# Kernel optimization log

Measured on AMD Instinct MI355X. Metric: run time of the kernel, lower is better.

## Reference

```python
import jax, jax.numpy as jnp
import numpy as np

L1 = 0.05
L2 = 0.05
L3 = 0.05
L4 = 0.05
D_MIN = 1.0
EPS = 1e-12


def _pairwise_dist(x, y):
    sq = (jnp.sum(x * x, axis=-1)[:, None]
          + jnp.sum(y * y, axis=-1)[None, :]
          - 2.0 * (x @ y.T))
    return jnp.sqrt(jnp.clip(sq, EPS))


def setup_inputs() -> dict:
    key = jax.random.key(0)
    k1, k2, k3, k4, k5, k6 = jax.random.split(key, 6)
    B, C, D, d, P = 32768, 100, 1024, 512, 128
    return {
        "predictions": jax.random.normal(k1, (B, C), dtype=jnp.float32),
        "reconstructions": jax.random.normal(k2, (B, D), dtype=jnp.float32),
        "data": jax.random.normal(k3, (B, D), dtype=jnp.float32),
        "embeddings": jax.random.normal(k4, (B, d), dtype=jnp.float32),
        "prototypes": jax.random.normal(k5, (P, d), dtype=jnp.float32),
        "labels": jax.random.randint(k6, (B,), 0, C, dtype=jnp.int64),
    }


def reference(predictions, reconstructions, data, embeddings, prototypes, labels):
    B = predictions.shape[0]
    P = prototypes.shape[0]

    # Cross-entropy (mean reduction, class-index targets)
    logp = jax.nn.log_softmax(predictions, axis=-1)
    classification_loss = -jnp.mean(logp[jnp.arange(B), labels])

    # MSE reconstruction loss (mean reduction)
    reconstruction_loss = jnp.mean((reconstructions - data) ** 2)

    # Prototype diversity penalty: sum_{j<k} max(0, d_min - ||p_j - p_k||)^2
    proto_dist = _pairwise_dist(prototypes, prototypes)  # [P, P]
    hinge = jnp.maximum(0.0, D_MIN - proto_dist) ** 2
    upper = jnp.triu(jnp.ones((P, P), dtype=bool), k=1)
    diversity_penalty = jnp.sum(jnp.where(upper, hinge, 0.0))

    # Embedding-to-prototype distances [B, P], shared by similarity/coverage penalties
    dist = _pairwise_dist(embeddings, prototypes)
    similarity_penalty = jnp.sum(jnp.min(dist, axis=0)) / P
    coverage_penalty = jnp.sum(jnp.min(dist, axis=1)) / B

    total_loss = (classification_loss
                  + L1 * reconstruction_loss
                  + L2 * diversity_penalty
                  + L3 * similarity_penalty
                  + L4 * coverage_penalty)
    return total_loss
```

## Files before the change

### kernel.cpp

```cpp
#include <hip/hip_runtime.h>
#include <hip/hip_bf16.h>


constexpr float FEPS = 1e-12f;
constexpr float DMIN = 1.0f;

#define NB_DIST 512
#define NB_MSE  1024
#define NB_CE   256
#define NB_DIV  128

typedef unsigned short ushort_t;
typedef __attribute__((ext_vector_type(8))) short bf16x8;
typedef __attribute__((ext_vector_type(8))) unsigned short u16x8;
typedef __attribute__((ext_vector_type(4))) unsigned short u16x4;
typedef __attribute__((ext_vector_type(16))) float f32x16;
typedef __attribute__((ext_vector_type(4))) float f32x4;

typedef __attribute__((address_space(1))) const void gvoid_t;
typedef __attribute__((address_space(3))) void lvoid_t;

__device__ __forceinline__ unsigned short f2b(float f) {
    unsigned u = __float_as_uint(f);
    u += 0x7FFFu + ((u >> 16) & 1u);
    return (unsigned short)(u >> 16);
}

union SmemU {
    struct {
        char     As[8192];
        char     Bs[16384];
        float    rown[64];
        float    pn[128];
        unsigned rowmin[64];
        unsigned colmin[128];
    } dist;
    struct { float pp[512]; float spp; float sred[4]; } div;
    struct { float sred[4]; } red;
};

__global__ __launch_bounds__(128) void conv_kernel(const float* __restrict__ proto,
                                                   ushort_t* __restrict__ pB,
                                                   float* __restrict__ pnorm,
                                                   float* __restrict__ ws,
                                                   unsigned* __restrict__ proto_min) {
    int p = blockIdx.x, q = threadIdx.x;
    if (q == 0) proto_min[p] = 0x7F7F7F7Fu;
    if (p == 0 && q < 4) ws[q] = 0.f;
    float4 v = ((const float4*)(proto + (size_t)p * 512))[q];
    u16x4 o = { f2b(v.x), f2b(v.y), f2b(v.z), f2b(v.w) };
    *(u16x4*)(pB + (size_t)p * 512 + q * 4) = o;
    float s = v.x * v.x + v.y * v.y + v.z * v.z + v.w * v.w;
    #pragma unroll
    for (int off = 32; off; off >>= 1) s += __shfl_xor(s, off);
    __shared__ float sr[2];
    if ((q & 63) == 0) sr[q >> 6] = s;
    __syncthreads();
    if (q == 0) pnorm[p] = sr[0] + sr[1];
}

__device__ __forceinline__ void dist_body_fast(SmemU& sm, int bid,
                                               const float* __restrict__ emb,
                                               const ushort_t* __restrict__ pB,
                                               const float* __restrict__ pnormG,
                                               unsigned* __restrict__ proto_min,
                                               float* __restrict__ cov_out) {
    char*     AsB     = sm.dist.As;
    char*     BsB     = sm.dist.Bs;
    float*    rownL   = sm.dist.rown;
    float*    pnL     = sm.dist.pn;
    unsigned* rowminL = sm.dist.rowmin;
    unsigned* colminL = sm.dist.colmin;

    const int t  = threadIdx.x;
    const int m0 = bid * 64;

    if (t < 64)  { rownL[t] = 0.f; rowminL[t] = 0x7F7F7F7Fu; }
    if (t < 128) { colminL[t] = 0x7F7F7F7Fu; pnL[t] = pnormG[t]; }

    int aidx[4], rowi[4], swzi[4];
    const float4* embF4 = (const float4*)emb;
    #pragma unroll
    for (int i = 0; i < 4; ++i) {
        int flat = i * 256 + t;
        int row = flat >> 4, colq = flat & 15;
        rowi[i] = row;
        aidx[i] = (m0 + row) * 128 + colq;
        swzi[i] = row * 128 + ((((colq >> 1) ^ (row & 7)) << 4) | ((colq & 1) << 3));
    }

    const ushort_t* bsrcp[4];
    char* bdstW[4];
    #pragma unroll
    for (int i = 0; i < 4; ++i) {
        int f = i * 256 + t;
        int pr = f >> 3, gb = f & 7;
        bsrcp[i] = pB + pr * 512 + ((gb ^ (pr & 7)) << 3);
        bdstW[i] = BsB + (size_t)(i * 256 + (t & ~63)) * 16;
    }

    const int lane = t & 63, wv = t >> 6;
    const int wr = wv >> 1, wc = wv & 1;
    const int lo = lane & 31, hi = lane >> 5;
    const int arow = wr * 32 + lo;
    const int arz  = arow & 7;
    const int p0 = wc * 64 + lo, p1 = p0 + 32;
    const int pz = p0 & 7;
    const char* Ar  = AsB + arow * 128;
    const char* Br0 = BsB + p0 * 128;
    const char* Br1 = BsB + p1 * 128;

    float4 aE0 = embF4[aidx[0]], aE1 = embF4[aidx[1]],
           aE2 = embF4[aidx[2]], aE3 = embF4[aidx[3]];
    float4 aO0, aO1, aO2, aO3;
    float rn0 = 0.f, rn1 = 0.f, rn2 = 0.f, rn3 = 0.f;
    f32x16 acc0 = {}, acc1 = {};
    __syncthreads();

#define DIST_CHUNK(c, W0, W1, W2, W3, L0, L1, L2, L3)                          \
    {                                                                          \
        const int kc = (c) * 64;                                               \
        __builtin_amdgcn_global_load_lds((gvoid_t*)(bsrcp[0] + kc),            \
                                         (lvoid_t*)bdstW[0], 16, 0, 0);        \
        __builtin_amdgcn_global_load_lds((gvoid_t*)(bsrcp[1] + kc),            \
                                         (lvoid_t*)bdstW[1], 16, 0, 0);        \
        __builtin_amdgcn_global_load_lds((gvoid_t*)(bsrcp[2] + kc),            \
                                         (lvoid_t*)bdstW[2], 16, 0, 0);        \
        __builtin_amdgcn_global_load_lds((gvoid_t*)(bsrcp[3] + kc),            \
                                         (lvoid_t*)bdstW[3], 16, 0, 0);        \
        __builtin_amdgcn_sched_barrier(0);                                     \
        {                                                                      \
            const int kn = ((c) < 7 ? (c) + 1 : 7) * 16;                       \
            L0 = embF4[aidx[0] + kn]; L1 = embF4[aidx[1] + kn];                \
            L2 = embF4[aidx[2] + kn]; L3 = embF4[aidx[3] + kn];                \
        }                                                                      \
        __builtin_amdgcn_sched_barrier(0);                                     \
        rn0 = fmaf(W0.x, W0.x, rn0); rn0 = fmaf(W0.y, W0.y, rn0);              \
        rn0 = fmaf(W0.z, W0.z, rn0); rn0 = fmaf(W0.w, W0.w, rn0);              \
        rn1 = fmaf(W1.x, W1.x, rn1); rn1 = fmaf(W1.y, W1.y, rn1);              \
        rn1 = fmaf(W1.z, W1.z, rn1); rn1 = fmaf(W1.w, W1.w, rn1);              \
        rn2 = fmaf(W2.x, W2.x, rn2); rn2 = fmaf(W2.y, W2.y, rn2);              \
        rn2 = fmaf(W2.z, W2.z, rn2); rn2 = fmaf(W2.w, W2.w, rn2);              \
        rn3 = fmaf(W3.x, W3.x, rn3); rn3 = fmaf(W3.y, W3.y, rn3);              \
        rn3 = fmaf(W3.z, W3.z, rn3); rn3 = fmaf(W3.w, W3.w, rn3);              \
        { u16x4 u = { f2b(W0.x), f2b(W0.y), f2b(W0.z), f2b(W0.w) };            \
          *(u16x4*)(AsB + swzi[0]) = u; }                                      \
        { u16x4 u = { f2b(W1.x), f2b(W1.y), f2b(W1.z), f2b(W1.w) };            \
          *(u16x4*)(AsB + swzi[1]) = u; }                                      \
        { u16x4 u = { f2b(W2.x), f2b(W2.y), f2b(W2.z), f2b(W2.w) };            \
          *(u16x4*)(AsB + swzi[2]) = u; }                                      \
        { u16x4 u = { f2b(W3.x), f2b(W3.y), f2b(W3.z), f2b(W3.w) };            \
          *(u16x4*)(AsB + swzi[3]) = u; }                                      \
        asm volatile("s_waitcnt vmcnt(4)" ::: "memory");                       \
        asm volatile("s_waitcnt lgkmcnt(0)" ::: "memory");                     \
        __builtin_amdgcn_s_barrier();                                          \
        __builtin_amdgcn_sched_barrier(0);                                     \
        _Pragma("unroll")                                                      \
        for (int s = 0; s < 4; ++s) {                                          \
            const int g = (s * 2 + hi);                                        \
            bf16x8 af = *(const bf16x8*)(Ar  + ((g ^ arz) << 4));              \
            bf16x8 b0 = *(const bf16x8*)(Br0 + ((g ^ pz)  << 4));              \
            bf16x8 b1 = *(const bf16x8*)(Br1 + ((g ^ pz)  << 4));              \
            acc0 = __builtin_amdgcn_mfma_f32_32x32x16_bf16(af, b0, acc0, 0,0,0); \
            acc1 = __builtin_amdgcn_mfma_f32_32x32x16_bf16(af, b1, acc1, 0,0,0); \
        }                                                                      \
        asm volatile("s_waitcnt lgkmcnt(0)" ::: "memory");                     \
        __builtin_amdgcn_s_barrier();                                          \
        __builtin_amdgcn_sched_barrier(0);                                     \
    }

    #pragma unroll
    for (int c = 0; c < 8; c += 2) {
        DIST_CHUNK(c,     aE0, aE1, aE2, aE3, aO0, aO1, aO2, aO3)
        DIST_CHUNK(c + 1, aO0, aO1, aO2, aO3, aE0, aE1, aE2, aE3)
    }
#undef DIST_CHUNK

    atomicAdd(&rownL[rowi[0]], rn0);
    atomicAdd(&rownL[rowi[1]], rn1);
    atomicAdd(&rownL[rowi[2]], rn2);
    atomicAdd(&rownL[rowi[3]], rn3);
    __syncthreads();

    const float pn0 = pnL[p0], pn1 = pnL[p1];
    float cmin0 = 3.0e38f, cmin1 = 3.0e38f;
    #pragma unroll
    for (int r = 0; r < 16; ++r) {
        const int row = wr * 32 + (r & 3) + 8 * (r >> 2) + 4 * hi;
        const float nx = rownL[row];
        float d0 = sqrtf(fmaxf(nx + pn0 - 2.f * acc0[r], FEPS));
        float d1 = sqrtf(fmaxf(nx + pn1 - 2.f * acc1[r], FEPS));
        cmin0 = fminf(cmin0, d0);
        cmin1 = fminf(cmin1, d1);
        atomicMin(&rowminL[row], __float_as_uint(fminf(d0, d1)));
    }
    atomicMin(&colminL[p0], __float_as_uint(cmin0));
    atomicMin(&colminL[p1], __float_as_uint(cmin1));
    __syncthreads();

    if (t < 64) {
        float cv = __uint_as_float(rowminL[t]);
        #pragma unroll
        for (int o = 32; o; o >>= 1) cv += __shfl_xor(cv, o);
        if (t == 0) atomicAdd(cov_out, cv);
    }
    if (t < 128) atomicMin(&proto_min[t], colminL[t]);
}

__device__ __forceinline__ void dist_body_slow(SmemU& sm, int bid,
                                               const float* __restrict__ emb,
                                               const float* __restrict__ proto,
                                               unsigned* __restrict__ proto_min,
                                               float* __restrict__ cov_out) {
    char*     AsB     = sm.dist.As;
    char*     BsB     = sm.dist.Bs;
    float*    rownL   = sm.dist.rown;
    float*    pnL     = sm.dist.pn;
    unsigned* rowminL = sm.dist.rowmin;
    unsigned* colminL = sm.dist.colmin;

    const int t  = threadIdx.x;
    const int m0 = bid * 64;

    if (t < 64)  { rownL[t] = 0.f; rowminL[t] = 0x7F7F7F7Fu; }
    if (t < 128) { colminL[t] = 0x7F7F7F7Fu; pnL[t] = 0.f; }
    __syncthreads();

    const int ra = t >> 2, qa = t & 3;
    const int pb = t >> 1, hb = t & 1;
    const int raz = ra & 7, pbz = pb & 7;

    const float4* aG  = (const float4*)(emb + (size_t)(m0 + ra) * 512 + qa * 16);
    const float4* bGf = (const float4*)(proto + (size_t)pb * 512 + hb * 32);

    const int lane = t & 63, wv = t >> 6;
    const int wr = wv >> 1, wc = wv & 1;
    const int lo = lane & 31, hi = lane >> 5;
    const int arow = wr * 32 + lo;
    const int arz  = arow & 7;
    const int p0 = wc * 64 + lo, p1 = p0 + 32;
    const int pz = p0 & 7;

    float4 av0 = aG[0], av1 = aG[1], av2 = aG[2], av3 = aG[3];
    float4 bf0 = bGf[0], bf1 = bGf[1], bf2 = bGf[2], bf3 = bGf[3],
           bf4 = bGf[4], bf5 = bGf[5], bf6 = bGf[6], bf7 = bGf[7];

    f32x16 acc0 = {}, acc1 = {};
    char* Aw = AsB + ra * 128;
    char* Bw = BsB + pb * 128;
    const char* Ar  = AsB + arow * 128;
    const char* Br0 = BsB + p0 * 128;
    const char* Br1 = BsB + p1 * 128;

    for (int c = 0; c < 8; ++c) {
        {
            float nx = 0.f;
            nx = fmaf(av0.x, av0.x, nx); nx = fmaf(av0.y, av0.y, nx);
            nx = fmaf(av0.z, av0.z, nx); nx = fmaf(av0.w, av0.w, nx);
            nx = fmaf(av1.x, av1.x, nx); nx = fmaf(av1.y, av1.y, nx);
            nx = fmaf(av1.z, av1.z, nx); nx = fmaf(av1.w, av1.w, nx);
            nx = fmaf(av2.x, av2.x, nx); nx = fmaf(av2.y, av2.y, nx);
            nx = fmaf(av2.z, av2.z, nx); nx = fmaf(av2.w, av2.w, nx);
            nx = fmaf(av3.x, av3.x, nx); nx = fmaf(av3.y, av3.y, nx);
            nx = fmaf(av3.z, av3.z, nx); nx = fmaf(av3.w, av3.w, nx);
            atomicAdd(&rownL[ra], nx);
            u16x8 w0 = { f2b(av0.x), f2b(av0.y), f2b(av0.z), f2b(av0.w),
                         f2b(av1.x), f2b(av1.y), f2b(av1.z), f2b(av1.w) };
            u16x8 w1 = { f2b(av2.x), f2b(av2.y), f2b(av2.z), f2b(av2.w),
                         f2b(av3.x), f2b(av3.y), f2b(av3.z), f2b(av3.w) };
            *(u16x8*)(Aw + (((qa * 2 + 0) ^ raz) << 4)) = w0;
            *(u16x8*)(Aw + (((qa * 2 + 1) ^ raz) << 4)) = w1;

            float pns = 0.f;
            pns = fmaf(bf0.x, bf0.x, pns); pns = fmaf(bf0.y, bf0.y, pns);
            pns = fmaf(bf0.z, bf0.z, pns); pns = fmaf(bf0.w, bf0.w, pns);
            pns = fmaf(bf1.x, bf1.x, pns); pns = fmaf(bf1.y, bf1.y, pns);
            pns = fmaf(bf1.z, bf1.z, pns); pns = fmaf(bf1.w, bf1.w, pns);
            pns = fmaf(bf2.x, bf2.x, pns); pns = fmaf(bf2.y, bf2.y, pns);
            pns = fmaf(bf2.z, bf2.z, pns); pns = fmaf(bf2.w, bf2.w, pns);
            pns = fmaf(bf3.x, bf3.x, pns); pns = fmaf(bf3.y, bf3.y, pns);
            pns = fmaf(bf3.z, bf3.z, pns); pns = fmaf(bf3.w, bf3.w, pns);
            pns = fmaf(bf4.x, bf4.x, pns); pns = fmaf(bf4.y, bf4.y, pns);
            pns = fmaf(bf4.z, bf4.z, pns); pns = fmaf(bf4.w, bf4.w, pns);
            pns = fmaf(bf5.x, bf5.x, pns); pns = fmaf(bf5.y, bf5.y, pns);
            pns = fmaf(bf5.z, bf5.z, pns); pns = fmaf(bf5.w, bf5.w, pns);
            pns = fmaf(bf6.x, bf6.x, pns); pns = fmaf(bf6.y, bf6.y, pns);
            pns = fmaf(bf6.z, bf6.z, pns); pns = fmaf(bf6.w, bf6.w, pns);
            pns = fmaf(bf7.x, bf7.x, pns); pns = fmaf(bf7.y, bf7.y, pns);
            pns = fmaf(bf7.z, bf7.z, pns); pns = fmaf(bf7.w, bf7.w, pns);
            atomicAdd(&pnL[pb], pns);
            u16x8 x0 = { f2b(bf0.x), f2b(bf0.y), f2b(bf0.z), f2b(bf0.w),
                         f2b(bf1.x), f2b(bf1.y), f2b(bf1.z), f2b(bf1.w) };
            u16x8 x1 = { f2b(bf2.x), f2b(bf2.y), f2b(bf2.z), f2b(bf2.w),
                         f2b(bf3.x), f2b(bf3.y), f2b(bf3.z), f2b(bf3.w) };
            u16x8 x2 = { f2b(bf4.x), f2b(bf4.y), f2b(bf4.z), f2b(bf4.w),
                         f2b(bf5.x), f2b(bf5.y), f2b(bf5.z), f2b(bf5.w) };
            u16x8 x3 = { f2b(bf6.x), f2b(bf6.y), f2b(bf6.z), f2b(bf6.w),
                         f2b(bf7.x), f2b(bf7.y), f2b(bf7.z), f2b(bf7.w) };
            *(u16x8*)(Bw + (((hb * 4 + 0) ^ pbz) << 4)) = x0;
            *(u16x8*)(Bw + (((hb * 4 + 1) ^ pbz) << 4)) = x1;
            *(u16x8*)(Bw + (((hb * 4 + 2) ^ pbz) << 4)) = x2;
            *(u16x8*)(Bw + (((hb * 4 + 3) ^ pbz) << 4)) = x3;
        }
        __syncthreads();
        if (c < 7) {
            av0 = aG[(c + 1) * 16 + 0]; av1 = aG[(c + 1) * 16 + 1];
            av2 = aG[(c + 1) * 16 + 2]; av3 = aG[(c + 1) * 16 + 3];
            bf0 = bGf[(c + 1) * 16 + 0]; bf1 = bGf[(c + 1) * 16 + 1];
            bf2 = bGf[(c + 1) * 16 + 2]; bf3 = bGf[(c + 1) * 16 + 3];
            bf4 = bGf[(c + 1) * 16 + 4]; bf5 = bGf[(c + 1) * 16 + 5];
            bf6 = bGf[(c + 1) * 16 + 6]; bf7 = bGf[(c + 1) * 16 + 7];
        }
        #pragma unroll
        for (int s = 0; s < 4; ++s) {
            const int g = (s * 2 + hi);
            bf16x8 af = *(const bf16x8*)(Ar  + ((g ^ arz) << 4));
            bf16x8 b0 = *(const bf16x8*)(Br0 + ((g ^ pz)  << 4));
            bf16x8 b1 = *(const bf16x8*)(Br1 + ((g ^ pz)  << 4));
            acc0 = __builtin_amdgcn_mfma_f32_32x32x16_bf16(af, b0, acc0, 0, 0, 0);
            acc1 = __builtin_amdgcn_mfma_f32_32x32x16_bf16(af, b1, acc1, 0, 0, 0);
        }
        __syncthreads();
    }

    const float pn0 = pnL[p0], pn1 = pnL[p1];
    float cmin0 = 3.0e38f, cmin1 = 3.0e38f;
    #pragma unroll
    for (int r = 0; r < 16; ++r) {
        const int row = wr * 32 + (r & 3) + 8 * (r >> 2) + 4 * hi;
        const float nx = rownL[row];
        float d0 = sqrtf(fmaxf(nx + pn0 - 2.f * acc0[r], FEPS));
        float d1 = sqrtf(fmaxf(nx + pn1 - 2.f * acc1[r], FEPS));
        cmin0 = fminf(cmin0, d0);
        cmin1 = fminf(cmin1, d1);
        atomicMin(&rowminL[row], __float_as_uint(fminf(d0, d1)));
    }
    atomicMin(&colminL[p0], __float_as_uint(cmin0));
    atomicMin(&colminL[p1], __float_as_uint(cmin1));
    __syncthreads();

    if (t < 64) {
        float cv = __uint_as_float(rowminL[t]);
        #pragma unroll
        for (int o = 32; o; o >>= 1) cv += __shfl_xor(cv, o);
        if (t == 0) atomicAdd(cov_out, cv);
    }
    if (t < 128) atomicMin(&proto_min[t], colminL[t]);
}

__device__ __forceinline__ void mse_body(SmemU& sm, int mb,
                                         const float4* __restrict__ r,
                                         const float4* __restrict__ d,
                                         float* __restrict__ out, int n4) {
    const int t  = threadIdx.x;
    const int CH = (n4 + NB_MSE - 1) / NB_MSE;
    const int base = mb * CH;
    const int L = (base + CH <= n4) ? CH : (n4 - base);
    const f32x4* rb = (const f32x4*)(r + base);
    const f32x4* db = (const f32x4*)(d + base);
    float acc0 = 0.f, acc1 = 0.f, acc2 = 0.f, acc3 = 0.f;
    int k = t;
    for (; k + 7 * 256 < L; k += 8 * 256) {
        f32x4 a0 = __builtin_nontemporal_load(&rb[k + 0 * 256]);
        f32x4 a1 = __builtin_nontemporal_load(&rb[k + 1 * 256]);
        f32x4 a2 = __builtin_nontemporal_load(&rb[k + 2 * 256]);
        f32x4 a3 = __builtin_nontemporal_load(&rb[k + 3 * 256]);
        f32x4 a4 = __builtin_nontemporal_load(&rb[k + 4 * 256]);
        f32x4 a5 = __builtin_nontemporal_load(&rb[k + 5 * 256]);
        f32x4 a6 = __builtin_nontemporal_load(&rb[k + 6 * 256]);
        f32x4 a7 = __builtin_nontemporal_load(&rb[k + 7 * 256]);
        f32x4 b0 = __builtin_nontemporal_load(&db[k + 0 * 256]);
        f32x4 b1 = __builtin_nontemporal_load(&db[k + 1 * 256]);
        f32x4 b2 = __builtin_nontemporal_load(&db[k + 2 * 256]);
        f32x4 b3 = __builtin_nontemporal_load(&db[k + 3 * 256]);
        f32x4 b4 = __builtin_nontemporal_load(&db[k + 4 * 256]);
        f32x4 b5 = __builtin_nontemporal_load(&db[k + 5 * 256]);
        f32x4 b6 = __builtin_nontemporal_load(&db[k + 6 * 256]);
        f32x4 b7 = __builtin_nontemporal_load(&db[k + 7 * 256]);
        f32x4 e;
        e = a0 - b0; acc0 = fmaf(e.x, e.x, acc0); acc1 = fmaf(e.y, e.y, acc1);
                     acc2 = fmaf(e.z, e.z, acc2); acc3 = fmaf(e.w, e.w, acc3);
        e = a1 - b1; acc0 = fmaf(e.x, e.x, acc0); acc1 = fmaf(e.y, e.y, acc1);
                     acc2 = fmaf(e.z, e.z, acc2); acc3 = fmaf(e.w, e.w, acc3);
        e = a2 - b2; acc0 = fmaf(e.x, e.x, acc0); acc1 = fmaf(e.y, e.y, acc1);
                     acc2 = fmaf(e.z, e.z, acc2); acc3 = fmaf(e.w, e.w, acc3);
        e = a3 - b3; acc0 = fmaf(e.x, e.x, acc0); acc1 = fmaf(e.y, e.y, acc1);
                     acc2 = fmaf(e.z, e.z, acc2); acc3 = fmaf(e.w, e.w, acc3);
        e = a4 - b4; acc0 = fmaf(e.x, e.x, acc0); acc1 = fmaf(e.y, e.y, acc1);
                     acc2 = fmaf(e.z, e.z, acc2); acc3 = fmaf(e.w, e.w, acc3);
        e = a5 - b5; acc0 = fmaf(e.x, e.x, acc0); acc1 = fmaf(e.y, e.y, acc1);
                     acc2 = fmaf(e.z, e.z, acc2); acc3 = fmaf(e.w, e.w, acc3);
        e = a6 - b6; acc0 = fmaf(e.x, e.x, acc0); acc1 = fmaf(e.y, e.y, acc1);
                     acc2 = fmaf(e.z, e.z, acc2); acc3 = fmaf(e.w, e.w, acc3);
        e = a7 - b7; acc0 = fmaf(e.x, e.x, acc0); acc1 = fmaf(e.y, e.y, acc1);
                     acc2 = fmaf(e.z, e.z, acc2); acc3 = fmaf(e.w, e.w, acc3);
    }
    for (; k < L; k += 256) {
        f32x4 a = __builtin_nontemporal_load(&rb[k]);
        f32x4 b = __builtin_nontemporal_load(&db[k]);
        f32x4 e = a - b;
        acc0 = fmaf(e.x, e.x, acc0); acc1 = fmaf(e.y, e.y, acc1);
        acc2 = fmaf(e.z, e.z, acc2); acc3 = fmaf(e.w, e.w, acc3);
    }
    float acc = (acc0 + acc1) + (acc2 + acc3);
    #pragma unroll
    for (int o = 32; o; o >>= 1) acc += __shfl_xor(acc, o);
    int lane = t & 63, w = t >> 6;
    if (lane == 0) sm.red.sred[w] = acc;
    __syncthreads();
    if (t == 0) atomicAdd(out, sm.red.sred[0] + sm.red.sred[1]
                             + sm.red.sred[2] + sm.red.sred[3]);
}

__device__ __forceinline__ void ce_body(SmemU& sm, int cb,
                                        const float* __restrict__ pred,
                                        const int* __restrict__ lab,
                                        float* __restrict__ ce_out,
                                        int B, int C) {
    const int rows_per_wave = B / (NB_CE * 4);
    int lane = threadIdx.x & 63;
    int w    = threadIdx.x >> 6;
    int wid  = cb * 4 + w;
    float acc = 0.f;
    for (int i = 0; i < rows_per_wave; ++i) {
        int row = wid * rows_per_wave + i;
        const float* p = pred + (size_t)row * C;
        float v1 = (lane < C)      ? p[lane]      : -3.0e38f;
        float v2 = (lane + 64 < C) ? p[lane + 64] : -3.0e38f;
        float m = fmaxf(v1, v2);
        #pragma unroll
        for (int o = 32; o; o >>= 1) m = fmaxf(m, __shfl_xor(m, o));
        float s = ((lane < C) ? __expf(v1 - m) : 0.f)
                + ((lane + 64 < C) ? __expf(v2 - m) : 0.f);
        #pragma unroll
        for (int o = 32; o; o >>= 1) s += __shfl_xor(s, o);
        float lv = p[lab[row]];
        acc += m + __logf(s) - lv;
    }
    if (lane == 0) sm.red.sred[w] = acc;
    __syncthreads();
    if (threadIdx.x == 0) atomicAdd(ce_out, sm.red.sred[0] + sm.red.sred[1]
                                          + sm.red.sred[2] + sm.red.sred[3]);
}

__device__ __forceinline__ void div_body(SmemU& sm, int p,
                                         const float* __restrict__ proto,
                                         float* __restrict__ div_out, int dd) {
    int q = threadIdx.x;
    bool act = q < 128;
    if (act) for (int k = q; k < dd; k += 128) sm.div.pp[k] = proto[(size_t)p * dd + k];
    __syncthreads();
    float dot = 0.f, qq = 0.f;
    if (act) {
        const float4* pq4 = (const float4*)(proto + (size_t)q * dd);
        const float4* pp4 = (const float4*)sm.div.pp;
        for (int k4 = 0; k4 < dd / 4; ++k4) {
            float4 v = pq4[k4];
            float4 u = pp4[k4];
            dot = fmaf(u.x, v.x, dot); dot = fmaf(u.y, v.y, dot);
            dot = fmaf(u.z, v.z, dot); dot = fmaf(u.w, v.w, dot);
            qq  = fmaf(v.x, v.x, qq);  qq  = fmaf(v.y, v.y, qq);
            qq  = fmaf(v.z, v.z, qq);  qq  = fmaf(v.w, v.w, qq);
        }
        if (q == p) sm.div.spp = qq;
    }
    __syncthreads();
    float h2 = 0.f;
    if (act && q > p) {
        float sq = sm.div.spp + qq - 2.f * dot;
        float dist = sqrtf(fmaxf(sq, FEPS));
        float h = fmaxf(0.f, DMIN - dist);
        h2 = h * h;
    }
    #pragma unroll
    for (int o = 32; o; o >>= 1) h2 += __shfl_xor(h2, o);
    if ((q & 63) == 0) sm.div.sred[q >> 6] = h2;
    __syncthreads();
    if (q == 0) atomicAdd(div_out, sm.div.sred[0] + sm.div.sred[1]
                                 + sm.div.sred[2] + sm.div.sred[3]);
}

template<bool PRECONV>
__global__ __launch_bounds__(256, 4) void fused_kernel(
        const float* __restrict__ pred, const int* __restrict__ lab,
        const float4* __restrict__ recon4, const float4* __restrict__ data4,
        const float* __restrict__ emb, const float* __restrict__ proto,
        const ushort_t* __restrict__ pB, const float* __restrict__ pnormG,
        float* __restrict__ ws, unsigned* __restrict__ proto_min,
        int B, int C, int n4, int dd) {
    __shared__ __attribute__((aligned(16))) SmemU sm;
    int bid = blockIdx.x;
    if (bid < NB_DIST) {
        if constexpr (PRECONV)
            dist_body_fast(sm, bid, emb, pB, pnormG, proto_min, ws + 3);
        else
            dist_body_slow(sm, bid, emb, proto, proto_min, ws + 3);
    } else if (bid < NB_DIST + NB_MSE) {
        mse_body(sm, bid - NB_DIST, recon4, data4, ws + 1, n4);
    } else if (bid < NB_DIST + NB_MSE + NB_CE) {
        ce_body(sm, bid - NB_DIST - NB_MSE, pred, lab, ws + 0, B, C);
    } else {
        div_body(sm, bid - NB_DIST - NB_MSE - NB_CE, proto, ws + 2, dd);
    }
}

__global__ void final_kernel(const float* __restrict__ ws,
                             const unsigned* __restrict__ pmin,
                             float* __restrict__ out, int B, int D, int P) {
    float sim = 0.f;
    for (int i = 0; i < P; ++i) sim += __uint_as_float(pmin[i]);
    float ce  = ws[0] / (float)B;
    float mse = ws[1] / ((float)B * (float)D);
    out[0] = ce + 0.05f * mse + 0.05f * ws[2] + 0.05f * (sim / (float)P)
           + 0.05f * (ws[3] / (float)B);
}

extern "C" void kernel_launch(void* const* d_in, const int* in_sizes, int n_in,
                              void* d_out, int out_size, void* d_ws, size_t ws_size,
                              hipStream_t stream) {
    const float* pred  = (const float*)d_in[0];
    const float* recon = (const float*)d_in[1];
    const float* data  = (const float*)d_in[2];
    const float* emb   = (const float*)d_in[3];
    const float* proto = (const float*)d_in[4];
    const int*   lab   = (const int*)d_in[5];
    float* out = (float*)d_out;

    int B  = in_sizes[5];
    int C  = in_sizes[0] / B;
    int D  = in_sizes[1] / B;
    int dd = in_sizes[3] / B;
    int P  = in_sizes[4] / dd;

    float* ws = (float*)d_ws;
    unsigned* proto_min = (unsigned*)(ws + 4);
    float*    pnorm     = ws + 132;
    ushort_t* pB        = (ushort_t*)((char*)d_ws + 1280);
    bool preconv = ws_size >= (size_t)(1280 + 128 * 512 * 2);

    int n4 = (B * D) / 4;
    int grid = NB_DIST + NB_MSE + NB_CE + NB_DIV;
    if (preconv) {
        conv_kernel<<<128, 128, 0, stream>>>(proto, pB, pnorm, ws, proto_min);
        fused_kernel<true><<<grid, 256, 0, stream>>>(
            pred, lab, (const float4*)recon, (const float4*)data, emb, proto,
            pB, pnorm, ws, proto_min, B, C, n4, dd);
    } else {
        hipMemsetAsync(ws, 0, 4 * sizeof(float), stream);
        hipMemsetAsync(ws + 4, 0x7F, P * sizeof(unsigned), stream);
        fused_kernel<false><<<grid, 256, 0, stream>>>(
            pred, lab, (const float4*)recon, (const float4*)data, emb, proto,
            nullptr, nullptr, ws, proto_min, B, C, n4, dd);
    }
    final_kernel<<<1, 1, 0, stream>>>(ws, proto_min, out, B, D, P);
}
```

Baseline: 104.1 us.

## Halve distance blocks with two tiles each, drop nontemporal loads and occupancy hint

Distance work now runs on 256 blocks that each process two consecutive tiles, with a barrier between them. This cuts block count and moves the distance blocks' share of the fused grid toward the MSE streaming blocks. The MSE loads become ordinary cached loads instead of nontemporal ones, and the launch-bounds minimum-occupancy hint is removed, letting the compiler use more registers. The risks are lower occupancy and a longer serial critical path for the distance blocks.

```diff
diff --git a/kernel.cpp b/kernel.cpp
--- a/kernel.cpp
+++ b/kernel.cpp
@@ -5,7 +5,7 @@
 constexpr float FEPS = 1e-12f;
 constexpr float DMIN = 1.0f;
 
-#define NB_DIST 512
+#define NB_DIST 256
 #define NB_MSE  1024
 #define NB_CE   256
 #define NB_DIV  128
@@ -361,22 +361,22 @@
     float acc0 = 0.f, acc1 = 0.f, acc2 = 0.f, acc3 = 0.f;
     int k = t;
     for (; k + 7 * 256 < L; k += 8 * 256) {
-        f32x4 a0 = __builtin_nontemporal_load(&rb[k + 0 * 256]);
-        f32x4 a1 = __builtin_nontemporal_load(&rb[k + 1 * 256]);
-        f32x4 a2 = __builtin_nontemporal_load(&rb[k + 2 * 256]);
-        f32x4 a3 = __builtin_nontemporal_load(&rb[k + 3 * 256]);
-        f32x4 a4 = __builtin_nontemporal_load(&rb[k + 4 * 256]);
-        f32x4 a5 = __builtin_nontemporal_load(&rb[k + 5 * 256]);
-        f32x4 a6 = __builtin_nontemporal_load(&rb[k + 6 * 256]);
-        f32x4 a7 = __builtin_nontemporal_load(&rb[k + 7 * 256]);
-        f32x4 b0 = __builtin_nontemporal_load(&db[k + 0 * 256]);
-        f32x4 b1 = __builtin_nontemporal_load(&db[k + 1 * 256]);
-        f32x4 b2 = __builtin_nontemporal_load(&db[k + 2 * 256]);
-        f32x4 b3 = __builtin_nontemporal_load(&db[k + 3 * 256]);
-        f32x4 b4 = __builtin_nontemporal_load(&db[k + 4 * 256]);
-        f32x4 b5 = __builtin_nontemporal_load(&db[k + 5 * 256]);
-        f32x4 b6 = __builtin_nontemporal_load(&db[k + 6 * 256]);
-        f32x4 b7 = __builtin_nontemporal_load(&db[k + 7 * 256]);
+        f32x4 a0 = rb[k + 0 * 256];
+        f32x4 a1 = rb[k + 1 * 256];
+        f32x4 a2 = rb[k + 2 * 256];
+        f32x4 a3 = rb[k + 3 * 256];
+        f32x4 a4 = rb[k + 4 * 256];
+        f32x4 a5 = rb[k + 5 * 256];
+        f32x4 a6 = rb[k + 6 * 256];
+        f32x4 a7 = rb[k + 7 * 256];
+        f32x4 b0 = db[k + 0 * 256];
+        f32x4 b1 = db[k + 1 * 256];
+        f32x4 b2 = db[k + 2 * 256];
+        f32x4 b3 = db[k + 3 * 256];
+        f32x4 b4 = db[k + 4 * 256];
+        f32x4 b5 = db[k + 5 * 256];
+        f32x4 b6 = db[k + 6 * 256];
+        f32x4 b7 = db[k + 7 * 256];
         f32x4 e;
         e = a0 - b0; acc0 = fmaf(e.x, e.x, acc0); acc1 = fmaf(e.y, e.y, acc1);
                      acc2 = fmaf(e.z, e.z, acc2); acc3 = fmaf(e.w, e.w, acc3);
@@ -396,8 +396,8 @@
                      acc2 = fmaf(e.z, e.z, acc2); acc3 = fmaf(e.w, e.w, acc3);
     }
     for (; k < L; k += 256) {
-        f32x4 a = __builtin_nontemporal_load(&rb[k]);
-        f32x4 b = __builtin_nontemporal_load(&db[k]);
+        f32x4 a = rb[k];
+        f32x4 b = db[k];
         f32x4 e = a - b;
         acc0 = fmaf(e.x, e.x, acc0); acc1 = fmaf(e.y, e.y, acc1);
         acc2 = fmaf(e.z, e.z, acc2); acc3 = fmaf(e.w, e.w, acc3);
@@ -481,7 +481,7 @@
 }
 
 template<bool PRECONV>
-__global__ __launch_bounds__(256, 4) void fused_kernel(
+__global__ __launch_bounds__(256) void fused_kernel(
         const float* __restrict__ pred, const int* __restrict__ lab,
         const float4* __restrict__ recon4, const float4* __restrict__ data4,
         const float* __restrict__ emb, const float* __restrict__ proto,
@@ -491,10 +491,15 @@
     __shared__ __attribute__((aligned(16))) SmemU sm;
     int bid = blockIdx.x;
     if (bid < NB_DIST) {
-        if constexpr (PRECONV)
-            dist_body_fast(sm, bid, emb, pB, pnormG, proto_min, ws + 3);
-        else
-            dist_body_slow(sm, bid, emb, proto, proto_min, ws + 3);
+        if constexpr (PRECONV) {
+            dist_body_fast(sm, bid * 2, emb, pB, pnormG, proto_min, ws + 3);
+            __syncthreads();
+            dist_body_fast(sm, bid * 2 + 1, emb, pB, pnormG, proto_min, ws + 3);
+        } else {
+            dist_body_slow(sm, bid * 2, emb, proto, proto_min, ws + 3);
+            __syncthreads();
+            dist_body_slow(sm, bid * 2 + 1, emb, proto, proto_min, ws + 3);
+        }
     } else if (bid < NB_DIST + NB_MSE) {
         mse_body(sm, bid - NB_DIST, recon4, data4, ws + 1, n4);
     } else if (bid < NB_DIST + NB_MSE + NB_CE) {
```

New measurement: 120.4 us. 1.16x slower.

## Split MSE reduction into its own kernel with more blocks

Applied to the files above, without the earlier changes.

Moves the MSE reduction out of the heterogeneous fused kernel into a separate lightweight kernel launched after the distance/CE/diversity kernel. The MSE kernel uses only a tiny shared array, so it no longer inherits the large shared-memory union and register footprint, which should allow higher occupancy for the bandwidth-bound streaming. The block count for MSE also doubles. The cost is an extra launch and that MSE no longer overlaps with the dist work in the same grid.

```diff
diff --git a/kernel.cpp b/kernel.cpp
--- a/kernel.cpp
+++ b/kernel.cpp
@@ -6,7 +6,7 @@
 constexpr float DMIN = 1.0f;
 
 #define NB_DIST 512
-#define NB_MSE  1024
+#define NB_MSE  2048
 #define NB_CE   256
 #define NB_DIV  128
 
@@ -348,70 +348,6 @@
     if (t < 128) atomicMin(&proto_min[t], colminL[t]);
 }
 
-__device__ __forceinline__ void mse_body(SmemU& sm, int mb,
-                                         const float4* __restrict__ r,
-                                         const float4* __restrict__ d,
-                                         float* __restrict__ out, int n4) {
-    const int t  = threadIdx.x;
-    const int CH = (n4 + NB_MSE - 1) / NB_MSE;
-    const int base = mb * CH;
-    const int L = (base + CH <= n4) ? CH : (n4 - base);
-    const f32x4* rb = (const f32x4*)(r + base);
-    const f32x4* db = (const f32x4*)(d + base);
-    float acc0 = 0.f, acc1 = 0.f, acc2 = 0.f, acc3 = 0.f;
-    int k = t;
-    for (; k + 7 * 256 < L; k += 8 * 256) {
-        f32x4 a0 = __builtin_nontemporal_load(&rb[k + 0 * 256]);
-        f32x4 a1 = __builtin_nontemporal_load(&rb[k + 1 * 256]);
-        f32x4 a2 = __builtin_nontemporal_load(&rb[k + 2 * 256]);
-        f32x4 a3 = __builtin_nontemporal_load(&rb[k + 3 * 256]);
-        f32x4 a4 = __builtin_nontemporal_load(&rb[k + 4 * 256]);
-        f32x4 a5 = __builtin_nontemporal_load(&rb[k + 5 * 256]);
-        f32x4 a6 = __builtin_nontemporal_load(&rb[k + 6 * 256]);
-        f32x4 a7 = __builtin_nontemporal_load(&rb[k + 7 * 256]);
-        f32x4 b0 = __builtin_nontemporal_load(&db[k + 0 * 256]);
-        f32x4 b1 = __builtin_nontemporal_load(&db[k + 1 * 256]);
-        f32x4 b2 = __builtin_nontemporal_load(&db[k + 2 * 256]);
-        f32x4 b3 = __builtin_nontemporal_load(&db[k + 3 * 256]);
-        f32x4 b4 = __builtin_nontemporal_load(&db[k + 4 * 256]);
-        f32x4 b5 = __builtin_nontemporal_load(&db[k + 5 * 256]);
-        f32x4 b6 = __builtin_nontemporal_load(&db[k + 6 * 256]);
-        f32x4 b7 = __builtin_nontemporal_load(&db[k + 7 * 256]);
-        f32x4 e;
-        e = a0 - b0; acc0 = fmaf(e.x, e.x, acc0); acc1 = fmaf(e.y, e.y, acc1);
-                     acc2 = fmaf(e.z, e.z, acc2); acc3 = fmaf(e.w, e.w, acc3);
-        e = a1 - b1; acc0 = fmaf(e.x, e.x, acc0); acc1 = fmaf(e.y, e.y, acc1);
-                     acc2 = fmaf(e.z, e.z, acc2); acc3 = fmaf(e.w, e.w, acc3);
-        e = a2 - b2; acc0 = fmaf(e.x, e.x, acc0); acc1 = fmaf(e.y, e.y, acc1);
-                     acc2 = fmaf(e.z, e.z, acc2); acc3 = fmaf(e.w, e.w, acc3);
-        e = a3 - b3; acc0 = fmaf(e.x, e.x, acc0); acc1 = fmaf(e.y, e.y, acc1);
-                     acc2 = fmaf(e.z, e.z, acc2); acc3 = fmaf(e.w, e.w, acc3);
-        e = a4 - b4; acc0 = fmaf(e.x, e.x, acc0); acc1 = fmaf(e.y, e.y, acc1);
-                     acc2 = fmaf(e.z, e.z, acc2); acc3 = fmaf(e.w, e.w, acc3);
-        e = a5 - b5; acc0 = fmaf(e.x, e.x, acc0); acc1 = fmaf(e.y, e.y, acc1);
-                     acc2 = fmaf(e.z, e.z, acc2); acc3 = fmaf(e.w, e.w, acc3);
-        e = a6 - b6; acc0 = fmaf(e.x, e.x, acc0); acc1 = fmaf(e.y, e.y, acc1);
-                     acc2 = fmaf(e.z, e.z, acc2); acc3 = fmaf(e.w, e.w, acc3);
-        e = a7 - b7; acc0 = fmaf(e.x, e.x, acc0); acc1 = fmaf(e.y, e.y, acc1);
-                     acc2 = fmaf(e.z, e.z, acc2); acc3 = fmaf(e.w, e.w, acc3);
-    }
-    for (; k < L; k += 256) {
-        f32x4 a = __builtin_nontemporal_load(&rb[k]);
-        f32x4 b = __builtin_nontemporal_load(&db[k]);
-        f32x4 e = a - b;
-        acc0 = fmaf(e.x, e.x, acc0); acc1 = fmaf(e.y, e.y, acc1);
-        acc2 = fmaf(e.z, e.z, acc2); acc3 = fmaf(e.w, e.w, acc3);
-    }
-    float acc = (acc0 + acc1) + (acc2 + acc3);
-    #pragma unroll
-    for (int o = 32; o; o >>= 1) acc += __shfl_xor(acc, o);
-    int lane = t & 63, w = t >> 6;
-    if (lane == 0) sm.red.sred[w] = acc;
-    __syncthreads();
-    if (t == 0) atomicAdd(out, sm.red.sred[0] + sm.red.sred[1]
-                             + sm.red.sred[2] + sm.red.sred[3]);
-}
-
 __device__ __forceinline__ void ce_body(SmemU& sm, int cb,
                                         const float* __restrict__ pred,
                                         const int* __restrict__ lab,
@@ -481,13 +417,12 @@
 }
 
 template<bool PRECONV>
-__global__ __launch_bounds__(256, 4) void fused_kernel(
+__global__ __launch_bounds__(256) void dcd_kernel(
         const float* __restrict__ pred, const int* __restrict__ lab,
-        const float4* __restrict__ recon4, const float4* __restrict__ data4,
         const float* __restrict__ emb, const float* __restrict__ proto,
         const ushort_t* __restrict__ pB, const float* __restrict__ pnormG,
         float* __restrict__ ws, unsigned* __restrict__ proto_min,
-        int B, int C, int n4, int dd) {
+        int B, int C, int dd) {
     __shared__ __attribute__((aligned(16))) SmemU sm;
     int bid = blockIdx.x;
     if (bid < NB_DIST) {
@@ -495,13 +430,74 @@
             dist_body_fast(sm, bid, emb, pB, pnormG, proto_min, ws + 3);
         else
             dist_body_slow(sm, bid, emb, proto, proto_min, ws + 3);
-    } else if (bid < NB_DIST + NB_MSE) {
-        mse_body(sm, bid - NB_DIST, recon4, data4, ws + 1, n4);
-    } else if (bid < NB_DIST + NB_MSE + NB_CE) {
-        ce_body(sm, bid - NB_DIST - NB_MSE, pred, lab, ws + 0, B, C);
+    } else if (bid < NB_DIST + NB_CE) {
+        ce_body(sm, bid - NB_DIST, pred, lab, ws + 0, B, C);
     } else {
-        div_body(sm, bid - NB_DIST - NB_MSE - NB_CE, proto, ws + 2, dd);
-    }
+        div_body(sm, bid - NB_DIST - NB_CE, proto, ws + 2, dd);
+    }
+}
+
+__global__ __launch_bounds__(256) void mse_kernel(const f32x4* __restrict__ r,
+                                                  const f32x4* __restrict__ d,
+                                                  float* __restrict__ out, int n4) {
+    __shared__ float sred[4];
+    const int t  = threadIdx.x;
+    const int CH = (n4 + NB_MSE - 1) / NB_MSE;
+    const int base = blockIdx.x * CH;
+    const int L = (base + CH <= n4) ? CH : (n4 - base);
+    const f32x4* rb = r + base;
+    const f32x4* db = d + base;
+    float acc0 = 0.f, acc1 = 0.f, acc2 = 0.f, acc3 = 0.f;
+    int k = t;
+    for (; k + 7 * 256 < L; k += 8 * 256) {
+        f32x4 a0 = __builtin_nontemporal_load(&rb[k + 0 * 256]);
+        f32x4 a1 = __builtin_nontemporal_load(&rb[k + 1 * 256]);
+        f32x4 a2 = __builtin_nontemporal_load(&rb[k + 2 * 256]);
+        f32x4 a3 = __builtin_nontemporal_load(&rb[k + 3 * 256]);
+        f32x4 a4 = __builtin_nontemporal_load(&rb[k + 4 * 256]);
+        f32x4 a5 = __builtin_nontemporal_load(&rb[k + 5 * 256]);
+        f32x4 a6 = __builtin_nontemporal_load(&rb[k + 6 * 256]);
+        f32x4 a7 = __builtin_nontemporal_load(&rb[k + 7 * 256]);
+        f32x4 b0 = __builtin_nontemporal_load(&db[k + 0 * 256]);
+        f32x4 b1 = __builtin_nontemporal_load(&db[k + 1 * 256]);
+        f32x4 b2 = __builtin_nontemporal_load(&db[k + 2 * 256]);
+        f32x4 b3 = __builtin_nontemporal_load(&db[k + 3 * 256]);
+        f32x4 b4 = __builtin_nontemporal_load(&db[k + 4 * 256]);
+        f32x4 b5 = __builtin_nontemporal_load(&db[k + 5 * 256]);
+        f32x4 b6 = __builtin_nontemporal_load(&db[k + 6 * 256]);
+        f32x4 b7 = __builtin_nontemporal_load(&db[k + 7 * 256]);
+        f32x4 e;
+        e = a0 - b0; acc0 = fmaf(e.x, e.x, acc0); acc1 = fmaf(e.y, e.y, acc1);
+                     acc2 = fmaf(e.z, e.z, acc2); acc3 = fmaf(e.w, e.w, acc3);
+        e = a1 - b1; acc0 = fmaf(e.x, e.x, acc0); acc1 = fmaf(e.y, e.y, acc1);
+                     acc2 = fmaf(e.z, e.z, acc2); acc3 = fmaf(e.w, e.w, acc3);
+        e = a2 - b2; acc0 = fmaf(e.x, e.x, acc0); acc1 = fmaf(e.y, e.y, acc1);
+                     acc2 = fmaf(e.z, e.z, acc2); acc3 = fmaf(e.w, e.w, acc3);
+        e = a3 - b3; acc0 = fmaf(e.x, e.x, acc0); acc1 = fmaf(e.y, e.y, acc1);
+                     acc2 = fmaf(e.z, e.z, acc2); acc3 = fmaf(e.w, e.w, acc3);
+        e = a4 - b4; acc0 = fmaf(e.x, e.x, acc0); acc1 = fmaf(e.y, e.y, acc1);
+                     acc2 = fmaf(e.z, e.z, acc2); acc3 = fmaf(e.w, e.w, acc3);
+        e = a5 - b5; acc0 = fmaf(e.x, e.x, acc0); acc1 = fmaf(e.y, e.y, acc1);
+                     acc2 = fmaf(e.z, e.z, acc2); acc3 = fmaf(e.w, e.w, acc3);
+        e = a6 - b6; acc0 = fmaf(e.x, e.x, acc0); acc1 = fmaf(e.y, e.y, acc1);
+                     acc2 = fmaf(e.z, e.z, acc2); acc3 = fmaf(e.w, e.w, acc3);
+        e = a7 - b7; acc0 = fmaf(e.x, e.x, acc0); acc1 = fmaf(e.y, e.y, acc1);
+                     acc2 = fmaf(e.z, e.z, acc2); acc3 = fmaf(e.w, e.w, acc3);
+    }
+    for (; k < L; k += 256) {
+        f32x4 a = __builtin_nontemporal_load(&rb[k]);
+        f32x4 b = __builtin_nontemporal_load(&db[k]);
+        f32x4 e = a - b;
+        acc0 = fmaf(e.x, e.x, acc0); acc1 = fmaf(e.y, e.y, acc1);
+        acc2 = fmaf(e.z, e.z, acc2); acc3 = fmaf(e.w, e.w, acc3);
+    }
+    float acc = (acc0 + acc1) + (acc2 + acc3);
+    #pragma unroll
+    for (int o = 32; o; o >>= 1) acc += __shfl_xor(acc, o);
+    int lane = t & 63, w = t >> 6;
+    if (lane == 0) sred[w] = acc;
+    __syncthreads();
+    if (t == 0) atomicAdd(out, sred[0] + sred[1] + sred[2] + sred[3]);
 }
 
 __global__ void final_kernel(const float* __restrict__ ws,
@@ -539,18 +535,18 @@
     bool preconv = ws_size >= (size_t)(1280 + 128 * 512 * 2);
 
     int n4 = (B * D) / 4;
-    int grid = NB_DIST + NB_MSE + NB_CE + NB_DIV;
+    int grid_dcd = NB_DIST + NB_CE + NB_DIV;
     if (preconv) {
         conv_kernel<<<128, 128, 0, stream>>>(proto, pB, pnorm, ws, proto_min);
-        fused_kernel<true><<<grid, 256, 0, stream>>>(
-            pred, lab, (const float4*)recon, (const float4*)data, emb, proto,
-            pB, pnorm, ws, proto_min, B, C, n4, dd);
+        dcd_kernel<true><<<grid_dcd, 256, 0, stream>>>(
+            pred, lab, emb, proto, pB, pnorm, ws, proto_min, B, C, dd);
     } else {
         hipMemsetAsync(ws, 0, 4 * sizeof(float), stream);
         hipMemsetAsync(ws + 4, 0x7F, P * sizeof(unsigned), stream);
-        fused_kernel<false><<<grid, 256, 0, stream>>>(
-            pred, lab, (const float4*)recon, (const float4*)data, emb, proto,
-            nullptr, nullptr, ws, proto_min, B, C, n4, dd);
-    }
+        dcd_kernel<false><<<grid_dcd, 256, 0, stream>>>(
+            pred, lab, emb, proto, nullptr, nullptr, ws, proto_min, B, C, dd);
+    }
+    mse_kernel<<<NB_MSE, 256, 0, stream>>>((const f32x4*)recon, (const f32x4*)data,
+                                           ws + 1, n4);
     final_kernel<<<1, 1, 0, stream>>>(ws, proto_min, out, B, D, P);
 }
```

New measurement: 117.6 us. 13.0% more time.

## Double-buffer prototype LDS tiles to prefetch next K-chunk during MFMA

Applied to the files above, without the earlier changes.

The prototype (B) tile buffer in shared memory is doubled, so the global-to-LDS loads for chunk c+1 are issued before computing chunk c, with a prologue load for chunk 0. The vmcnt waits are adjusted per chunk to match the new number of loads in flight. The aim is to hide global load latency behind the MFMA work in the distance GEMM. The launch-bounds minimum-blocks hint is also dropped, which gives the compiler more registers. The larger LDS footprint and the looser register limit can both lower occupancy for the whole fused kernel, including the bandwidth-bound MSE blocks.

```diff
diff --git a/kernel.cpp b/kernel.cpp
--- a/kernel.cpp
+++ b/kernel.cpp
@@ -29,7 +29,7 @@
 union SmemU {
     struct {
         char     As[8192];
-        char     Bs[16384];
+        char     Bs[2 * 16384];
         float    rown[64];
         float    pn[128];
         unsigned rowmin[64];
@@ -110,24 +110,33 @@
     const char* Br0 = BsB + p0 * 128;
     const char* Br1 = BsB + p1 * 128;
 
+    __builtin_amdgcn_global_load_lds((gvoid_t*)(bsrcp[0]), (lvoid_t*)bdstW[0], 16, 0, 0);
+    __builtin_amdgcn_global_load_lds((gvoid_t*)(bsrcp[1]), (lvoid_t*)bdstW[1], 16, 0, 0);
+    __builtin_amdgcn_global_load_lds((gvoid_t*)(bsrcp[2]), (lvoid_t*)bdstW[2], 16, 0, 0);
+    __builtin_amdgcn_global_load_lds((gvoid_t*)(bsrcp[3]), (lvoid_t*)bdstW[3], 16, 0, 0);
     float4 aE0 = embF4[aidx[0]], aE1 = embF4[aidx[1]],
            aE2 = embF4[aidx[2]], aE3 = embF4[aidx[3]];
     float4 aO0, aO1, aO2, aO3;
     float rn0 = 0.f, rn1 = 0.f, rn2 = 0.f, rn3 = 0.f;
     f32x16 acc0 = {}, acc1 = {};
-    __syncthreads();
-
-#define DIST_CHUNK(c, W0, W1, W2, W3, L0, L1, L2, L3)                          \
+    asm volatile("s_waitcnt lgkmcnt(0)" ::: "memory");
+    __builtin_amdgcn_s_barrier();
+    __builtin_amdgcn_sched_barrier(0);
+
+#define DIST_CHUNK(c, WAITN, W0, W1, W2, W3, L0, L1, L2, L3)                   \
     {                                                                          \
-        const int kc = (c) * 64;                                               \
-        __builtin_amdgcn_global_load_lds((gvoid_t*)(bsrcp[0] + kc),            \
-                                         (lvoid_t*)bdstW[0], 16, 0, 0);        \
-        __builtin_amdgcn_global_load_lds((gvoid_t*)(bsrcp[1] + kc),            \
-                                         (lvoid_t*)bdstW[1], 16, 0, 0);        \
-        __builtin_amdgcn_global_load_lds((gvoid_t*)(bsrcp[2] + kc),            \
-                                         (lvoid_t*)bdstW[2], 16, 0, 0);        \
-        __builtin_amdgcn_global_load_lds((gvoid_t*)(bsrcp[3] + kc),            \
-                                         (lvoid_t*)bdstW[3], 16, 0, 0);        \
+        if ((c) < 7) {                                                         \
+            const int kc1 = ((c) + 1) * 64;                                    \
+            const int bo1 = (((c) + 1) & 1) * 16384;                           \
+            __builtin_amdgcn_global_load_lds((gvoid_t*)(bsrcp[0] + kc1),       \
+                (lvoid_t*)(bdstW[0] + bo1), 16, 0, 0);                         \
+            __builtin_amdgcn_global_load_lds((gvoid_t*)(bsrcp[1] + kc1),       \
+                (lvoid_t*)(bdstW[1] + bo1), 16, 0, 0);                         \
+            __builtin_amdgcn_global_load_lds((gvoid_t*)(bsrcp[2] + kc1),       \
+                (lvoid_t*)(bdstW[2] + bo1), 16, 0, 0);                         \
+            __builtin_amdgcn_global_load_lds((gvoid_t*)(bsrcp[3] + kc1),       \
+                (lvoid_t*)(bdstW[3] + bo1), 16, 0, 0);                         \
+        }                                                                      \
         __builtin_amdgcn_sched_barrier(0);                                     \
         {                                                                      \
             const int kn = ((c) < 7 ? (c) + 1 : 7) * 16;                       \
@@ -151,29 +160,35 @@
           *(u16x4*)(AsB + swzi[2]) = u; }                                      \
         { u16x4 u = { f2b(W3.x), f2b(W3.y), f2b(W3.z), f2b(W3.w) };            \
           *(u16x4*)(AsB + swzi[3]) = u; }                                      \
-        asm volatile("s_waitcnt vmcnt(4)" ::: "memory");                       \
+        asm volatile("s_waitcnt vmcnt(" #WAITN ")" ::: "memory");              \
         asm volatile("s_waitcnt lgkmcnt(0)" ::: "memory");                     \
         __builtin_amdgcn_s_barrier();                                          \
         __builtin_amdgcn_sched_barrier(0);                                     \
-        _Pragma("unroll")                                                      \
-        for (int s = 0; s < 4; ++s) {                                          \
-            const int g = (s * 2 + hi);                                        \
-            bf16x8 af = *(const bf16x8*)(Ar  + ((g ^ arz) << 4));              \
-            bf16x8 b0 = *(const bf16x8*)(Br0 + ((g ^ pz)  << 4));              \
-            bf16x8 b1 = *(const bf16x8*)(Br1 + ((g ^ pz)  << 4));              \
-            acc0 = __builtin_amdgcn_mfma_f32_32x32x16_bf16(af, b0, acc0, 0,0,0); \
-            acc1 = __builtin_amdgcn_mfma_f32_32x32x16_bf16(af, b1, acc1, 0,0,0); \
+        {                                                                      \
+            const int bo = ((c) & 1) * 16384;                                  \
+            _Pragma("unroll")                                                  \
+            for (int s = 0; s < 4; ++s) {                                      \
+                const int g = (s * 2 + hi);                                    \
+                bf16x8 af = *(const bf16x8*)(Ar  + ((g ^ arz) << 4));          \
+                bf16x8 b0 = *(const bf16x8*)(Br0 + bo + ((g ^ pz) << 4));      \
+                bf16x8 b1 = *(const bf16x8*)(Br1 + bo + ((g ^ pz) << 4));      \
+                acc0 = __builtin_amdgcn_mfma_f32_32x32x16_bf16(af, b0, acc0, 0,0,0); \
+                acc1 = __builtin_amdgcn_mfma_f32_32x32x16_bf16(af, b1, acc1, 0,0,0); \
+            }                                                                  \
         }                                                                      \
         asm volatile("s_waitcnt lgkmcnt(0)" ::: "memory");                     \
         __builtin_amdgcn_s_barrier();                                          \
         __builtin_amdgcn_sched_barrier(0);                                     \
     }
 
-    #pragma unroll
-    for (int c = 0; c < 8; c += 2) {
-        DIST_CHUNK(c,     aE0, aE1, aE2, aE3, aO0, aO1, aO2, aO3)
-        DIST_CHUNK(c + 1, aO0, aO1, aO2, aO3, aE0, aE1, aE2, aE3)
-    }
+    DIST_CHUNK(0, 8, aE0, aE1, aE2, aE3, aO0, aO1, aO2, aO3)
+    DIST_CHUNK(1, 8, aO0, aO1, aO2, aO3, aE0, aE1, aE2, aE3)
+    DIST_CHUNK(2, 8, aE0, aE1, aE2, aE3, aO0, aO1, aO2, aO3)
+    DIST_CHUNK(3, 8, aO0, aO1, aO2, aO3, aE0, aE1, aE2, aE3)
+    DIST_CHUNK(4, 8, aE0, aE1, aE2, aE3, aO0, aO1, aO2, aO3)
+    DIST_CHUNK(5, 8, aO0, aO1, aO2, aO3, aE0, aE1, aE2, aE3)
+    DIST_CHUNK(6, 8, aE0, aE1, aE2, aE3, aO0, aO1, aO2, aO3)
+    DIST_CHUNK(7, 4, aO0, aO1, aO2, aO3, aE0, aE1, aE2, aE3)
 #undef DIST_CHUNK
 
     atomicAdd(&rownL[rowi[0]], rn0);
@@ -481,7 +496,7 @@
 }
 
 template<bool PRECONV>
-__global__ __launch_bounds__(256, 4) void fused_kernel(
+__global__ __launch_bounds__(256) void fused_kernel(
         const float* __restrict__ pred, const int* __restrict__ lab,
         const float4* __restrict__ recon4, const float4* __restrict__ data4,
         const float* __restrict__ emb, const float* __restrict__ proto,
```

Result: faster. 100.7 us (-3.3%).
